# Kernel tuning notes

Measured on AMD Instinct MI355X. Metric: run time of the kernel, lower is better.

## Reference

```python
import jax, jax.numpy as jnp
import numpy as np

TEMP_EPS = 1e-6


def setup_inputs() -> dict:
    key = jax.random.key(0)
    k1, k2, k3 = jax.random.split(key, 3)
    B, V = 128, 128256
    logits = jax.random.normal(k1, (B, V), dtype=jnp.float32)
    temperatures = jax.random.uniform(k2, (B,), dtype=jnp.float32)
    u = jax.random.uniform(k3, (B, V), dtype=jnp.float32)
    return {"logits": logits, "temperatures": temperatures, "u": u}


def reference(logits, temperatures, u):
    # Faithful vectorized version of the per-row loop:
    #   nan_to_num -> temperature scale -> softmax -> multinomial sample,
    # expressed as a single Gumbel-max over the batch (equivalent sampling
    # distribution), with greedy argmax where temp <= 1e-6.
    logits = jnp.nan_to_num(logits)                       # [B, V]
    greedy = jnp.argmax(logits, axis=-1)                  # [B]

    safe_temp = jnp.maximum(temperatures, TEMP_EPS)[:, None]  # [B, 1]
    scaled = logits / safe_temp                           # [B, V]

    # Gumbel-max trick: argmax(scaled + g), g ~ Gumbel(0,1), samples
    # exactly from softmax(scaled) == the multinomial in the original.
    uc = jnp.clip(u, 1e-10, 1.0 - 1e-7)
    gumbel = -jnp.log(-jnp.log(uc))                       # [B, V]
    sampled = jnp.argmax(scaled + gumbel, axis=-1)        # [B]

    use_greedy = temperatures <= TEMP_EPS                 # [B] bool
    return jnp.where(use_greedy, greedy, sampled)
```

## Files before the change

kernel.cpp:

```cpp
#include <hip/hip_runtime.h>
#include <cfloat>
#include <cstdint>


#define TEMP_EPS 1e-6f

static constexpr int V       = 128256;
static constexpr int V4      = V / 4;
static constexpr int SEGS    = 32;
static constexpr int SEG_V4  = V4 / SEGS;
static constexpr int TAIL    = SEG_V4 - 3 * 256;

__device__ __forceinline__ float nan_to_num_f(float x) {
    if (x != x) return 0.0f;
    return fminf(fmaxf(x, -FLT_MAX), FLT_MAX);
}

__device__ __forceinline__ unsigned long long pack_key(float v, int idx) {
    unsigned b = __float_as_uint(v);
    unsigned mask = (unsigned)(((int)b >> 31)) | 0x80000000u;
    b ^= mask;
    return ((unsigned long long)b << 32) | (unsigned)(~(unsigned)idx);
}

__device__ __forceinline__ unsigned long long umax64(unsigned long long a,
                                                     unsigned long long b) {
    return a > b ? a : b;
}

__global__ __launch_bounds__(256) void sampler_partial_kernel(
    const float* __restrict__ logits,
    const float* __restrict__ temps,
    const float* __restrict__ u,
    unsigned long long* __restrict__ partials) {
    const int row = blockIdx.y;
    const int seg = blockIdx.x;
    const int tid = threadIdx.x;

    const float temp = temps[row];
    const bool greedy = (temp <= TEMP_EPS);
    const float safe_temp = fmaxf(temp, TEMP_EPS);

    const float4* __restrict__ l4 = (const float4*)(logits + (size_t)row * V);
    const float4* __restrict__ u4 = (const float4*)(u + (size_t)row * V);

    const float UC_LO = 1e-10f;
    const float UC_HI = (float)(1.0 - 1e-7);

    const int base = seg * SEG_V4;

    int idx[4];
    idx[0] = base + tid;
    idx[1] = base + 256 + tid;
    idx[2] = base + 512 + tid;
    idx[3] = (tid < TAIL) ? (base + 768 + tid) : (base + tid);

    float4 lv[4], uv[4];
#pragma unroll
    for (int k = 0; k < 4; ++k) lv[k] = l4[idx[k]];
#pragma unroll
    for (int k = 0; k < 4; ++k) uv[k] = u4[idx[k]];

    unsigned long long key = 0ULL;

    if (greedy) {
#pragma unroll
        for (int k = 0; k < 4; ++k) {
            const int e = idx[k] * 4;
            float a = nan_to_num_f(lv[k].x);
            float b = nan_to_num_f(lv[k].y);
            float c = nan_to_num_f(lv[k].z);
            float d = nan_to_num_f(lv[k].w);
            key = umax64(key, pack_key(a, e + 0));
            key = umax64(key, pack_key(b, e + 1));
            key = umax64(key, pack_key(c, e + 2));
            key = umax64(key, pack_key(d, e + 3));
        }
    } else {
#pragma unroll
        for (int k = 0; k < 4; ++k) {
            const int e = idx[k] * 4;

            float l0 = nan_to_num_f(lv[k].x) / safe_temp;
            float l1 = nan_to_num_f(lv[k].y) / safe_temp;
            float l2 = nan_to_num_f(lv[k].z) / safe_temp;
            float l3 = nan_to_num_f(lv[k].w) / safe_temp;

            float c0 = fminf(fmaxf(uv[k].x, UC_LO), UC_HI);
            float c1 = fminf(fmaxf(uv[k].y, UC_LO), UC_HI);
            float c2 = fminf(fmaxf(uv[k].z, UC_LO), UC_HI);
            float c3 = fminf(fmaxf(uv[k].w, UC_LO), UC_HI);

            float g0 = -logf(-logf(c0));
            float g1 = -logf(-logf(c1));
            float g2 = -logf(-logf(c2));
            float g3 = -logf(-logf(c3));

            key = umax64(key, pack_key(l0 + g0, e + 0));
            key = umax64(key, pack_key(l1 + g1, e + 1));
            key = umax64(key, pack_key(l2 + g2, e + 2));
            key = umax64(key, pack_key(l3 + g3, e + 3));
        }
    }

    for (int o = 32; o > 0; o >>= 1)
        key = umax64(key, __shfl_down(key, o));

    __shared__ unsigned long long sdata[4];
    if ((tid & 63) == 0) sdata[tid >> 6] = key;
    __syncthreads();

    if (tid == 0) {
        for (int w = 1; w < 4; ++w) key = umax64(key, sdata[w]);
        partials[row * SEGS + seg] = key;
    }
}

__global__ __launch_bounds__(64) void sampler_reduce_kernel(
    const unsigned long long* __restrict__ partials,
    int* __restrict__ out) {
    const int row = blockIdx.x;
    const int t = threadIdx.x;
    unsigned long long key = (t < SEGS) ? partials[row * SEGS + t] : 0ULL;
    for (int o = 32; o > 0; o >>= 1)
        key = umax64(key, __shfl_down(key, o));
    if (t == 0)
        out[row] = (int)(~(unsigned)(key & 0xFFFFFFFFull));
}

extern "C" void kernel_launch(void* const* d_in, const int* in_sizes, int n_in,
                              void* d_out, int out_size, void* d_ws, size_t ws_size,
                              hipStream_t stream) {
    const float* logits = (const float*)d_in[0];
    const float* temps  = (const float*)d_in[1];
    const float* u      = (const float*)d_in[2];
    int* out = (int*)d_out;
    const int B = in_sizes[1];

    unsigned long long* partials = (unsigned long long*)d_ws;

    dim3 grid1(SEGS, B);
    hipLaunchKernelGGL(sampler_partial_kernel, grid1, dim3(256), 0, stream,
                       logits, temps, u, partials);
    hipLaunchKernelGGL(sampler_reduce_kernel, dim3(B), dim3(64), 0, stream,
                       partials, out);
}
```

Measured before the change: 148.6 us.

## Halve segments per row, double per-thread loads, use reciprocal temp and fast log

Cuts the segments per row from 32 to 16, so each thread now loads 8 float4 pairs instead of 4, which gives more bytes in flight per thread and fewer blocks. The division by temperature becomes a multiply by a precomputed reciprocal. The outer log of the Gumbel transform switches to the fast __logf intrinsic, and the max-combine is restructured as a tree. The greedy path no longer loads u. The risks are higher register pressure, lower occupancy, and small numeric differences that could flip argmax ties.

```diff
diff --git a/kernel.cpp b/kernel.cpp
--- a/kernel.cpp
+++ b/kernel.cpp
@@ -7,9 +7,10 @@
 
 static constexpr int V       = 128256;
 static constexpr int V4      = V / 4;
-static constexpr int SEGS    = 32;
+static constexpr int SEGS    = 16;
 static constexpr int SEG_V4  = V4 / SEGS;
-static constexpr int TAIL    = SEG_V4 - 3 * 256;
+static constexpr int ITERS   = 8;
+static constexpr int TAIL    = SEG_V4 - 7 * 256;
 
 __device__ __forceinline__ float nan_to_num_f(float x) {
     if (x != x) return 0.0f;
@@ -40,6 +41,7 @@
     const float temp = temps[row];
     const bool greedy = (temp <= TEMP_EPS);
     const float safe_temp = fmaxf(temp, TEMP_EPS);
+    const float inv_temp = 1.0f / safe_temp;
 
     const float4* __restrict__ l4 = (const float4*)(logits + (size_t)row * V);
     const float4* __restrict__ u4 = (const float4*)(u + (size_t)row * V);
@@ -49,57 +51,62 @@
 
     const int base = seg * SEG_V4;
 
-    int idx[4];
-    idx[0] = base + tid;
-    idx[1] = base + 256 + tid;
-    idx[2] = base + 512 + tid;
-    idx[3] = (tid < TAIL) ? (base + 768 + tid) : (base + tid);
-
-    float4 lv[4], uv[4];
+    int idx[ITERS];
 #pragma unroll
-    for (int k = 0; k < 4; ++k) lv[k] = l4[idx[k]];
-#pragma unroll
-    for (int k = 0; k < 4; ++k) uv[k] = u4[idx[k]];
+    for (int k = 0; k < ITERS - 1; ++k) idx[k] = base + k * 256 + tid;
+    idx[ITERS - 1] = (tid < TAIL) ? (base + (ITERS - 1) * 256 + tid) : (base + tid);
 
     unsigned long long key = 0ULL;
 
     if (greedy) {
+        float4 lv[ITERS];
 #pragma unroll
-        for (int k = 0; k < 4; ++k) {
+        for (int k = 0; k < ITERS; ++k) lv[k] = l4[idx[k]];
+#pragma unroll
+        for (int k = 0; k < ITERS; ++k) {
             const int e = idx[k] * 4;
-            float a = nan_to_num_f(lv[k].x);
-            float b = nan_to_num_f(lv[k].y);
-            float c = nan_to_num_f(lv[k].z);
-            float d = nan_to_num_f(lv[k].w);
-            key = umax64(key, pack_key(a, e + 0));
-            key = umax64(key, pack_key(b, e + 1));
-            key = umax64(key, pack_key(c, e + 2));
-            key = umax64(key, pack_key(d, e + 3));
+            unsigned long long k0 = pack_key(nan_to_num_f(lv[k].x), e + 0);
+            unsigned long long k1 = pack_key(nan_to_num_f(lv[k].y), e + 1);
+            unsigned long long k2 = pack_key(nan_to_num_f(lv[k].z), e + 2);
+            unsigned long long k3 = pack_key(nan_to_num_f(lv[k].w), e + 3);
+            key = umax64(key, umax64(umax64(k0, k1), umax64(k2, k3)));
         }
     } else {
+        float4 lv[ITERS], uv[ITERS];
 #pragma unroll
-        for (int k = 0; k < 4; ++k) {
+        for (int k = 0; k < ITERS; ++k) lv[k] = l4[idx[k]];
+#pragma unroll
+        for (int k = 0; k < ITERS; ++k) uv[k] = u4[idx[k]];
+
+#pragma unroll
+        for (int k = 0; k < ITERS; ++k) {
             const int e = idx[k] * 4;
 
-            float l0 = nan_to_num_f(lv[k].x) / safe_temp;
-            float l1 = nan_to_num_f(lv[k].y) / safe_temp;
-            float l2 = nan_to_num_f(lv[k].z) / safe_temp;
-            float l3 = nan_to_num_f(lv[k].w) / safe_temp;
+            float l0 = nan_to_num_f(lv[k].x) * inv_temp;
+            float l1 = nan_to_num_f(lv[k].y) * inv_temp;
+            float l2 = nan_to_num_f(lv[k].z) * inv_temp;
+            float l3 = nan_to_num_f(lv[k].w) * inv_temp;
 
             float c0 = fminf(fmaxf(uv[k].x, UC_LO), UC_HI);
             float c1 = fminf(fmaxf(uv[k].y, UC_LO), UC_HI);
             float c2 = fminf(fmaxf(uv[k].z, UC_LO), UC_HI);
             float c3 = fminf(fmaxf(uv[k].w, UC_LO), UC_HI);
 
-            float g0 = -logf(-logf(c0));
-            float g1 = -logf(-logf(c1));
-            float g2 = -logf(-logf(c2));
-            float g3 = -logf(-logf(c3));
+            float w0 = -logf(c0);
+            float w1 = -logf(c1);
+            float w2 = -logf(c2);
+            float w3 = -logf(c3);
 
-            key = umax64(key, pack_key(l0 + g0, e + 0));
-            key = umax64(key, pack_key(l1 + g1, e + 1));
-            key = umax64(key, pack_key(l2 + g2, e + 2));
-            key = umax64(key, pack_key(l3 + g3, e + 3));
+            float g0 = -__logf(w0);
+            float g1 = -__logf(w1);
+            float g2 = -__logf(w2);
+            float g3 = -__logf(w3);
+
+            unsigned long long k0 = pack_key(l0 + g0, e + 0);
+            unsigned long long k1 = pack_key(l1 + g1, e + 1);
+            unsigned long long k2 = pack_key(l2 + g2, e + 2);
+            unsigned long long k3 = pack_key(l3 + g3, e + 3);
+            key = umax64(key, umax64(umax64(k0, k1), umax64(k2, k3)));
         }
     }
 
```

Result: no change. 149.0 us (+0.3%).
